# Performance work log

Measured on AMD Instinct MI355X. Metric: run time of the kernel, lower is better.

Reference implementation:

```python
import jax, jax.numpy as jnp
import numpy as np

N_NODES = 100000
N_EDGES = 1600000
IN_SIZE, HID_SIZE, OUT_SIZE = 128, 64, 64


def _glorot(key, shape):
    lim = float(np.sqrt(6.0 / (shape[0] + shape[1])))
    return jax.random.uniform(key, shape, jnp.float32, -lim, lim)


def setup_inputs() -> dict:
    key = jax.random.key(0)
    ks = jax.random.split(key, 6)
    features = jax.random.normal(ks[0], (N_NODES, IN_SIZE), jnp.float32)
    src = jax.random.randint(ks[1], (N_EDGES,), 0, N_NODES)
    dst = jax.random.randint(ks[2], (N_EDGES,), 0, N_NODES)
    return {
        "features": features,
        "W0": _glorot(ks[3], (IN_SIZE, HID_SIZE)),
        "b0": jnp.zeros((HID_SIZE,), jnp.float32),
        "W1": _glorot(ks[4], (HID_SIZE, HID_SIZE)),
        "b1": jnp.zeros((HID_SIZE,), jnp.float32),
        "W2": _glorot(ks[5], (HID_SIZE, OUT_SIZE)),
        "b2": jnp.zeros((OUT_SIZE,), jnp.float32),
        "src": src,
        "dst": dst,
    }


def reference(features, W0, b0, W1, b1, W2, b2, src, dst):
    # DGL GraphConv with norm='both': h' = relu(D_in^{-1/2} A D_out^{-1/2} h W + b)
    # Dropout layers are identity in eval mode (deterministic baseline).
    N = features.shape[0]
    ones = jnp.ones(src.shape, features.dtype)
    deg_out = jax.ops.segment_sum(ones, src, num_segments=N)
    deg_in = jax.ops.segment_sum(ones, dst, num_segments=N)
    norm_src = jnp.where(deg_out > 0, deg_out, 1.0) ** -0.5  # [N]
    norm_dst = jnp.where(deg_in > 0, deg_in, 1.0) ** -0.5    # [N]

    def layer(h, W, b):
        h = h * norm_src[:, None]          # source-side degree norm
        m = (h @ W)[src]                   # project first (in >= out), then gather [E, d_out]
        agg = jax.ops.segment_sum(m, dst, num_segments=N)  # scatter-add to destinations
        return jax.nn.relu(agg * norm_dst[:, None] + b)

    h = layer(features, W0, b0)
    h = layer(h, W1, b1)
    return layer(h, W2, b2)
```

## Files before the change

### kernel.cpp

```cpp
#include <hip/hip_runtime.h>
#include <hip/hip_bf16.h>

typedef __hip_bfloat16 bf16;
typedef __attribute__((ext_vector_type(8))) short bf16x8;
typedef __attribute__((ext_vector_type(8))) unsigned short u16x8;
typedef __attribute__((ext_vector_type(4))) float f32x4;
typedef __attribute__((ext_vector_type(4))) int i32x4;
typedef __attribute__((ext_vector_type(4))) short s16x4;

__device__ __forceinline__ float b2f(unsigned short u) {
  return __uint_as_float(((unsigned)u) << 16);
}
__device__ __forceinline__ unsigned short f2b(float x) {
  bf16 h = __float2bfloat16(x);
  return *reinterpret_cast<unsigned short*>(&h);
}

__global__ void k_passA(const int* __restrict__ src, const int* __restrict__ dst, int E,
                        int nbuck, int M, int* __restrict__ counts,
                        const unsigned short* __restrict__ raw, int* __restrict__ flag) {
  if (blockIdx.x == 256) {
    __shared__ int sbad, snz;
    const int t = threadIdx.x;
    if (t == 0) { sbad = 0; snz = 0; }
    __syncthreads();
    const unsigned short u = raw[t];
    const float a = fabsf(b2f(u));
    if (!(a < 100.f)) atomicAdd(&sbad, 1);
    if (((t & 1) == 0) && u != 0) atomicAdd(&snz, 1);
    __syncthreads();
    if (t == 0) flag[0] = (sbad == 0 && snz > 0) ? 1 : 0;
    return;
  }
  extern __shared__ int lh[];
  int* lh1 = lh;
  int* lh2 = lh + nbuck;
  const int t = threadIdx.x;
  for (int k = t; k < 2 * nbuck; k += 256) lh[k] = 0;
  __syncthreads();
  const int chunk = (E + 255) / 256;
  const int s = blockIdx.x * chunk;
  const int e = min(E, s + chunk);
  for (int i = s + t; i < e; i += 256) {
    atomicAdd(&lh1[dst[i] >> 8], 1);
    atomicAdd(&lh2[src[i] >> 8], 1);
  }
  __syncthreads();
  for (int k = t; k < nbuck; k += 256) {
    counts[k * 256 + blockIdx.x] = lh1[k];
    counts[M + k * 256 + blockIdx.x] = lh2[k];
  }
}

__global__ void k_scan1(const int* __restrict__ a, int M2, int* __restrict__ bsums) {
  __shared__ int sdata[256];
  int i = blockIdx.x * 256 + threadIdx.x;
  int v = (i < M2) ? a[i] : 0;
  sdata[threadIdx.x] = v;
  __syncthreads();
  for (int s = 128; s > 0; s >>= 1) {
    if (threadIdx.x < s) sdata[threadIdx.x] += sdata[threadIdx.x + s];
    __syncthreads();
  }
  if (threadIdx.x == 0) bsums[blockIdx.x] = sdata[0];
}

__global__ void k_scan2(int* __restrict__ bsums, int nb, int* __restrict__ rowStart,
                        int N, int E) {
  __shared__ int s[1024];
  const int t = threadIdx.x;
  const int v = (t < nb) ? bsums[t] : 0;
  s[t] = v;
  __syncthreads();
  for (int off = 1; off < 1024; off <<= 1) {
    int u = (t >= off) ? s[t - off] : 0;
    __syncthreads();
    s[t] += u;
    __syncthreads();
  }
  if (t < nb) bsums[t] = s[t] - v;
  if (t == 0) rowStart[N] = E;
}

__global__ void k_scan3(int* __restrict__ a, int M2, const int* __restrict__ bsums) {
  __shared__ int sdata[256];
  int i = blockIdx.x * 256 + threadIdx.x;
  int v = (i < M2) ? a[i] : 0;
  sdata[threadIdx.x] = v;
  __syncthreads();
  for (int off = 1; off < 256; off <<= 1) {
    int t = (threadIdx.x >= off) ? sdata[threadIdx.x - off] : 0;
    __syncthreads();
    sdata[threadIdx.x] += t;
    __syncthreads();
  }
  if (i < M2) a[i] = bsums[blockIdx.x] + sdata[threadIdx.x] - v;
}

__global__ void k_passC(const int* __restrict__ src, const int* __restrict__ dst, int E,
                        int nbuck, int M, const int* __restrict__ S,
                        int* __restrict__ tmp, unsigned char* __restrict__ tmp2) {
  extern __shared__ int cur[];
  int* cur1 = cur;
  int* cur2 = cur + nbuck;
  const int t = threadIdx.x;
  for (int k = t; k < nbuck; k += 256) {
    cur1[k] = S[k * 256 + blockIdx.x];
    cur2[k] = S[M + k * 256 + blockIdx.x];
  }
  __syncthreads();
  const int chunk = (E + 255) / 256;
  const int s = blockIdx.x * chunk;
  const int e = min(E, s + chunk);
  for (int i = s + t; i < e; i += 256) {
    const int sv = src[i];
    const int d = dst[i];
    const int pos1 = atomicAdd(&cur1[d >> 8], 1);
    tmp[pos1] = sv | ((d & 255) << 20);
    const int pos2 = atomicAdd(&cur2[sv >> 8], 1);
    tmp2[pos2 - E] = (unsigned char)(sv & 255);
  }
}

__global__ void k_passD(const int* __restrict__ tmp, const unsigned char* __restrict__ tmp2,
                        const int* __restrict__ S, int nbuck, int M, int N, int E,
                        int* __restrict__ rowStart, int* __restrict__ edgeSrc,
                        float* __restrict__ ns, float* __restrict__ nd) {
  __shared__ int h[256];
  __shared__ int ex[256];
  __shared__ int c[256];
  const int t = threadIdx.x;
  const int k = blockIdx.x;
  const int node = k * 256 + t;
  const int bs2 = S[M + k * 256] - E;
  const int be2 = (k + 1 < nbuck) ? (S[M + (k + 1) * 256] - E) : E;
  h[t] = 0;
  __syncthreads();
  for (int i = bs2 + t; i < be2; i += 256) atomicAdd(&h[tmp2[i]], 1);
  __syncthreads();
  if (node < N) {
    int dov = h[t];
    if (dov <= 0) dov = 1;
    ns[node] = rsqrtf((float)dov);
  }
  __syncthreads();
  const int bs = S[k * 256];
  const int be = (k + 1 < nbuck) ? S[(k + 1) * 256] : E;
  h[t] = 0;
  __syncthreads();
  for (int i = bs + t; i < be; i += 256) atomicAdd(&h[tmp[i] >> 20], 1);
  __syncthreads();
  const int cnt = h[t];
  ex[t] = cnt;
  __syncthreads();
  for (int off = 1; off < 256; off <<= 1) {
    int u = (t >= off) ? ex[t - off] : 0;
    __syncthreads();
    ex[t] += u;
    __syncthreads();
  }
  const int excl = ex[t] - cnt;
  if (node < N) {
    rowStart[node] = bs + excl;
    nd[node] = rsqrtf((float)(cnt > 0 ? cnt : 1));
  }
  c[t] = bs + excl;
  __syncthreads();
  for (int i = bs + t; i < be; i += 256) {
    const int v = tmp[i];
    const int pos = atomicAdd(&c[v >> 20], 1);
    edgeSrc[pos] = v & 0xFFFFF;
  }
}

__global__ void k_prepW(const void* __restrict__ W0, const void* __restrict__ W1,
                        const void* __restrict__ W2, const int* __restrict__ flag,
                        unsigned short* __restrict__ WT0, unsigned short* __restrict__ WT1,
                        unsigned short* __restrict__ WT2) {
  const bool isb = (*flag != 0);
  const int i = blockIdx.x * 256 + threadIdx.x;
  if (i < 8192) {
    const int n = i >> 7, k = i & 127;
    const float v = isb ? b2f(((const unsigned short*)W0)[k * 64 + n])
                        : ((const float*)W0)[k * 64 + n];
    WT0[i] = f2b(v);
  } else if (i < 12288) {
    const int j = i - 8192;
    const int n = j >> 6, k = j & 63;
    const float v = isb ? b2f(((const unsigned short*)W1)[k * 64 + n])
                        : ((const float*)W1)[k * 64 + n];
    WT1[j] = f2b(v);
  } else if (i < 16384) {
    const int j = i - 12288;
    const int n = j >> 6, k = j & 63;
    const float v = isb ? b2f(((const unsigned short*)W2)[k * 64 + n])
                        : ((const float*)W2)[k * 64 + n];
    WT2[j] = f2b(v);
  }
}

template <int K, bool FIRST, bool SCALE>
__device__ __forceinline__ void gemm_loadA(const void* hin, bool isb, int rowA,
                                           int quad, bf16x8* A) {
  constexpr int KT = K / 32;
  if (FIRST && !isb) {
    const float* hp = (const float*)hin + (size_t)rowA * K;
#pragma unroll
    for (int kt = 0; kt < KT; ++kt) {
      const float4 u0 = *(const float4*)(hp + kt * 32 + quad * 8);
      const float4 u1 = *(const float4*)(hp + kt * 32 + quad * 8 + 4);
      A[kt][0] = (short)f2b(u0.x); A[kt][1] = (short)f2b(u0.y);
      A[kt][2] = (short)f2b(u0.z); A[kt][3] = (short)f2b(u0.w);
      A[kt][4] = (short)f2b(u1.x); A[kt][5] = (short)f2b(u1.y);
      A[kt][6] = (short)f2b(u1.z); A[kt][7] = (short)f2b(u1.w);
    }
  } else {
    const unsigned short* hp = (const unsigned short*)hin + (size_t)rowA * K;
#pragma unroll
    for (int kt = 0; kt < KT; ++kt)
      A[kt] = *(const bf16x8*)(hp + kt * 32 + quad * 8);
  }
}

template <int K, bool FIRST, bool SCALE>
__global__ void __launch_bounds__(256) k_gemm(
    const void* __restrict__ hin, const unsigned short* __restrict__ WT,
    const int* __restrict__ flag, const float* __restrict__ norm_src,
    int N, unsigned short* __restrict__ out) {
  constexpr int KT = K / 32;
  constexpr int CST = 72;
  __shared__ unsigned short Cl[4][16 * CST];
  const bool isb = (*flag != 0);
  const int tid = threadIdx.x;
  const int lane = tid & 63;
  const int quad = lane >> 4;
  const int l16 = lane & 15;
  const int w = tid >> 6;
  unsigned short* myC = &Cl[w][0];

  bf16x8 Bf[KT][4];
#pragma unroll
  for (int kt = 0; kt < KT; ++kt)
#pragma unroll
    for (int nt = 0; nt < 4; ++nt)
      Bf[kt][nt] = *(const bf16x8*)(WT + (size_t)(nt * 16 + l16) * K + kt * 32 + quad * 8);

  const int wid = blockIdx.x * 4 + w;
  const int nw = gridDim.x * 4;
  const int G = (N + 15) >> 4;

  bf16x8 A0[KT], A1[KT];
  if (wid < G) {
    int r0 = (wid << 4) + l16;
    if (r0 >= N) r0 = N - 1;
    gemm_loadA<K, FIRST, SCALE>(hin, isb, r0, quad, A0);
  }
  for (int g = wid; g < G; g += nw) {
    if (g + nw < G) {
      int r1 = ((g + nw) << 4) + l16;
      if (r1 >= N) r1 = N - 1;
      gemm_loadA<K, FIRST, SCALE>(hin, isb, r1, quad, A1);
    }
    f32x4 acc[4] = {{0.f, 0.f, 0.f, 0.f}, {0.f, 0.f, 0.f, 0.f},
                    {0.f, 0.f, 0.f, 0.f}, {0.f, 0.f, 0.f, 0.f}};
#pragma unroll
    for (int kt = 0; kt < KT; ++kt) {
#pragma unroll
      for (int nt = 0; nt < 4; ++nt)
        acc[nt] = __builtin_amdgcn_mfma_f32_16x16x32_bf16(A0[kt], Bf[kt][nt], acc[nt], 0, 0, 0);
    }
    const int rowD = quad * 4;
#pragma unroll
    for (int r = 0; r < 4; ++r) {
      const int nodeW = (g << 4) + rowD + r;
      const float f = (SCALE && nodeW < N) ? norm_src[nodeW] : 1.0f;
#pragma unroll
      for (int nt = 0; nt < 4; ++nt)
        myC[(rowD + r) * CST + nt * 16 + l16] = f2b(SCALE ? acc[nt][r] * f : acc[nt][r]);
    }
    const int row2 = lane >> 2;
    const int c0 = (lane & 3) * 16;
    const int node = (g << 4) + row2;
    if (node < N) {
      const u16x8 v0 = *(const u16x8*)&myC[row2 * CST + c0];
      const u16x8 v1 = *(const u16x8*)&myC[row2 * CST + c0 + 8];
      *(u16x8*)(out + (size_t)node * 64 + c0) = v0;
      *(u16x8*)(out + (size_t)node * 64 + c0 + 8) = v1;
    }
#pragma unroll
    for (int kt = 0; kt < KT; ++kt) A0[kt] = A1[kt];
  }
}

__device__ __forceinline__ void agg_chunk_compute(unsigned trbase, int cb32, int lo,
                                                  unsigned span, int quad, f32x4* acc) {
  const int posbase = cb32 + (quad << 2);
  const unsigned u0 = (unsigned)(posbase - lo);
  bf16x8 Af;
#pragma unroll
  for (int j = 0; j < 8; ++j) {
    const unsigned off = (j < 4) ? (unsigned)j : (unsigned)(12 + j);
    Af[j] = ((u0 + off) < span) ? (short)0x3F80 : (short)0;
  }
  s16x4 t0[4], t1[4];
#pragma unroll
  for (int nt = 0; nt < 4; ++nt) {
    const unsigned a = trbase + (unsigned)(nt * 1024);
    asm volatile("ds_read_b64_tr_b16 %0, %1" : "=v"(t0[nt]) : "v"(a) : "memory");
    asm volatile("ds_read_b64_tr_b16 %0, %1 offset:512" : "=v"(t1[nt]) : "v"(a) : "memory");
  }
  asm volatile("s_waitcnt lgkmcnt(0)" ::: "memory");
  __builtin_amdgcn_sched_barrier(0);
#pragma unroll
  for (int nt = 0; nt < 4; ++nt) {
    bf16x8 Bf;
    Bf[0] = t0[nt][0]; Bf[1] = t0[nt][1]; Bf[2] = t0[nt][2]; Bf[3] = t0[nt][3];
    Bf[4] = t1[nt][0]; Bf[5] = t1[nt][1]; Bf[6] = t1[nt][2]; Bf[7] = t1[nt][3];
    acc[nt] = __builtin_amdgcn_mfma_f32_16x16x32_bf16(Af, Bf, acc[nt], 0, 0, 0);
  }
}

template <bool LAST>
__global__ void __launch_bounds__(256) k_aggregate(
    const unsigned short* __restrict__ proj,
    const int* __restrict__ edgeSrc, const int* __restrict__ rowStart,
    const float* __restrict__ norm_dst, const float* __restrict__ norm_src,
    const void* __restrict__ bias, const int* __restrict__ flag,
    int N, int E, void* __restrict__ outp) {
  __shared__ unsigned short lds[4][2048];
  const bool isb = (*flag != 0);
  const int tid = threadIdx.x;
  const int w = tid >> 6;
  const int lane = tid & 63;
  const int l16 = lane & 15;
  const int quad = lane >> 4;
  const int e32 = lane & 31;
  const int p = lane >> 5;

  const int wid = blockIdx.x * 4 + w;
  const int g0 = wid * 8;

  float bcol[4];
#pragma unroll
  for (int nt = 0; nt < 4; ++nt) {
    const int col = nt * 16 + l16;
    bcol[nt] = isb ? b2f(((const unsigned short*)bias)[col]) : ((const float*)bias)[col];
  }

  const int cb = rowStart[min(g0, N)];
  const int ce = rowStart[min(g0 + 8, N)];
  const int L = ce - cb;
  const int nch = (L + 31) >> 5;

  const int rsi = min(g0 + min(l16, 8), N);
  const int rsj = min(g0 + min(l16 + 1, 8), N);
  const int lo = rowStart[rsi];
  const unsigned span = (unsigned)(rowStart[rsj] - lo);

  int idxc[6];
#pragma unroll
  for (int t = 0; t < 6; ++t) {
    const int pos = min(cb + t * 32 + e32, E - 1);
    idxc[t] = edgeSrc[pos];
  }

  unsigned short* myl = &lds[w][0];
  unsigned wofs[4];
#pragma unroll
  for (int q = 0; q < 4; ++q) {
    const int n0 = p * 32 + q * 8;
    wofs[q] = (unsigned)((n0 >> 4) * 512 + e32 * 16 + (n0 & 15));
  }
  const unsigned trbase = (unsigned)(uintptr_t)myl + (unsigned)lane * 8u;

  f32x4 acc[4] = {{0.f, 0.f, 0.f, 0.f}, {0.f, 0.f, 0.f, 0.f},
                  {0.f, 0.f, 0.f, 0.f}, {0.f, 0.f, 0.f, 0.f}};

  i32x4 gb[4][4];
#define AGG_ISSUE(t, b)                                                         \
  {                                                                             \
    const unsigned short* rp = proj + (size_t)idxc[t] * 64 + p * 32;            \
    gb[b][0] = *(const i32x4*)(rp);                                             \
    gb[b][1] = *(const i32x4*)(rp + 8);                                         \
    gb[b][2] = *(const i32x4*)(rp + 16);                                        \
    gb[b][3] = *(const i32x4*)(rp + 24);                                        \
  }
  if (0 < nch) AGG_ISSUE(0, 0);
  if (1 < nch) AGG_ISSUE(1, 1);
  if (2 < nch) AGG_ISSUE(2, 2);
  if (3 < nch) AGG_ISSUE(3, 3);

#pragma unroll
  for (int tt = 0; tt < 6; ++tt) {
    if (tt < nch) {
#pragma unroll
      for (int q = 0; q < 4; ++q) *(i32x4*)(myl + wofs[q]) = gb[tt & 3][q];
      if (tt + 4 < 6 && tt + 4 < nch) AGG_ISSUE(tt + 4, tt & 3);
      asm volatile("s_waitcnt lgkmcnt(0)" ::: "memory");
      agg_chunk_compute(trbase, cb + tt * 32, lo, span, quad, acc);
    }
  }
  for (int t = 6; t < nch; ++t) {
    const int pos = min(cb + t * 32 + e32, E - 1);
    const int idx = edgeSrc[pos];
    const unsigned short* rp = proj + (size_t)idx * 64 + p * 32;
    i32x4 g4[4];
    g4[0] = *(const i32x4*)(rp);
    g4[1] = *(const i32x4*)(rp + 8);
    g4[2] = *(const i32x4*)(rp + 16);
    g4[3] = *(const i32x4*)(rp + 24);
#pragma unroll
    for (int q = 0; q < 4; ++q) *(i32x4*)(myl + wofs[q]) = g4[q];
    asm volatile("s_waitcnt lgkmcnt(0)" ::: "memory");
    agg_chunk_compute(trbase, cb + t * 32, lo, span, quad, acc);
  }
#undef AGG_ISSUE

  if (LAST && !isb) {
    float* fs = (float*)myl;
#pragma unroll
    for (int reg = 0; reg < 4; ++reg) {
      const int row = quad * 4 + reg;
      if (row < 8) {
        const int node = min(g0 + row, N - 1);
        const float nd = norm_dst[node];
#pragma unroll
        for (int nt = 0; nt < 4; ++nt)
          fs[row * 64 + nt * 16 + l16] = fmaxf(fmaf(acc[nt][reg], nd, bcol[nt]), 0.f);
      }
    }
    asm volatile("s_waitcnt lgkmcnt(0)" ::: "memory");
    __builtin_amdgcn_sched_barrier(0);
    const int r = lane >> 3;
    const int c0 = (lane & 7) * 8;
    const int node = g0 + r;
    if (node < N) {
      const float4 v0 = *(const float4*)&fs[r * 64 + c0];
      const float4 v1 = *(const float4*)&fs[r * 64 + c0 + 4];
      float* of = (float*)outp + (size_t)node * 64 + c0;
      *(float4*)of = v0;
      *(float4*)(of + 4) = v1;
    }
  } else {
#pragma unroll
    for (int reg = 0; reg < 4; ++reg) {
      const int row = quad * 4 + reg;
      if (row < 8) {
        const int node = min(g0 + row, N - 1);
        const float nd = norm_dst[node];
        const float esc = LAST ? 1.f : norm_src[node];
#pragma unroll
        for (int nt = 0; nt < 4; ++nt) {
          float x = fmaxf(fmaf(acc[nt][reg], nd, bcol[nt]), 0.f);
          if (!LAST) x *= esc;
          myl[row * 64 + nt * 16 + l16] = f2b(x);
        }
      }
    }
    asm volatile("s_waitcnt lgkmcnt(0)" ::: "memory");
    __builtin_amdgcn_sched_barrier(0);
    if (lane < 32) {
      const int r = lane >> 2;
      const int c0 = (lane & 3) * 16;
      const int node = g0 + r;
      if (node < N) {
        const u16x8 v0 = *(const u16x8*)&myl[r * 64 + c0];
        const u16x8 v1 = *(const u16x8*)&myl[r * 64 + c0 + 8];
        *(u16x8*)((unsigned short*)outp + (size_t)node * 64 + c0) = v0;
        *(u16x8*)((unsigned short*)outp + (size_t)node * 64 + c0 + 8) = v1;
      }
    }
  }
}

extern "C" void kernel_launch(void* const* d_in, const int* in_sizes, int n_in,
                              void* d_out, int out_size, void* d_ws, size_t ws_size,
                              hipStream_t stream) {
  const void* features = d_in[0];
  const void* W0 = d_in[1];
  const void* b0 = d_in[2];
  const void* W1 = d_in[3];
  const void* b1 = d_in[4];
  const void* W2 = d_in[5];
  const void* b2 = d_in[6];
  const int* src = (const int*)d_in[7];
  const int* dst = (const int*)d_in[8];
  const int N = in_sizes[0] / 128;
  const int E = in_sizes[7];
  const int NBUCK = (N + 255) >> 8;
  const int M = NBUCK * 256;
  const int M2 = 2 * M;

  char* w = (char*)d_ws;
  size_t off = 0;
  auto alloc = [&](size_t bytes) {
    void* p = w + off;
    off = (off + bytes + 255) & ~(size_t)255;
    return p;
  };
  int* flag = (int*)alloc(4);
  int* rowStart = (int*)alloc((size_t)(N + 1) * 4);
  int* counts = (int*)alloc((size_t)M2 * 4);
  int* bsums = (int*)alloc(1024 * 4);
  float* norm_src = (float*)alloc((size_t)N * 4);
  float* norm_dst = (float*)alloc((size_t)N * 4);
  int* tmp = (int*)alloc((size_t)E * 4);
  unsigned char* tmp2 = (unsigned char*)alloc((size_t)E);
  int* edgeSrc = (int*)alloc((size_t)E * 4);
  unsigned short* projA = (unsigned short*)alloc((size_t)N * 64 * 2);
  unsigned short* WT0 = (unsigned short*)alloc(64 * 128 * 2);
  unsigned short* WT1 = (unsigned short*)alloc(64 * 64 * 2);
  unsigned short* WT2 = (unsigned short*)alloc(64 * 64 * 2);
  unsigned short* hB = (unsigned short*)d_out;

  const size_t lds_nb = (size_t)NBUCK * 2 * 4;
  const int G16 = (N + 15) / 16;
  const int GB = (G16 + 7) / 8;

  k_passA<<<257, 256, lds_nb, stream>>>(src, dst, E, NBUCK, M, counts,
                                        (const unsigned short*)features, flag);
  const int NB2 = (M2 + 255) / 256;
  k_scan1<<<NB2, 256, 0, stream>>>(counts, M2, bsums);
  k_scan2<<<1, 1024, 0, stream>>>(bsums, NB2, rowStart, N, E);
  k_scan3<<<NB2, 256, 0, stream>>>(counts, M2, bsums);
  k_passC<<<256, 256, lds_nb, stream>>>(src, dst, E, NBUCK, M, counts, tmp, tmp2);
  k_passD<<<NBUCK, 256, 0, stream>>>(tmp, tmp2, counts, NBUCK, M, N, E,
                                     rowStart, edgeSrc, norm_src, norm_dst);
  k_prepW<<<64, 256, 0, stream>>>(W0, W1, W2, flag, WT0, WT1, WT2);

  const int AB = (((N + 7) / 8) + 3) / 4;
  k_gemm<128, true, true><<<GB, 256, 0, stream>>>(features, WT0, flag, norm_src, N, projA);
  k_aggregate<false><<<AB, 256, 0, stream>>>(projA, edgeSrc, rowStart, norm_dst, norm_src, b0, flag, N, E, hB);
  k_gemm<64, false, false><<<GB, 256, 0, stream>>>(hB, WT1, flag, nullptr, N, projA);
  k_aggregate<false><<<AB, 256, 0, stream>>>(projA, edgeSrc, rowStart, norm_dst, norm_src, b1, flag, N, E, hB);
  k_gemm<64, false, false><<<GB, 256, 0, stream>>>(hB, WT2, flag, nullptr, N, projA);
  k_aggregate<true><<<AB, 256, 0, stream>>>(projA, edgeSrc, rowStart, norm_dst, norm_src, b2, flag, N, E, d_out);
}
```

Measured before the change: 335.3 us.

## Fuse weight transpose into GEMM via LDS and shrink aggregate gather prefetch depth

Drops the separate weight-prep kernel. Each GEMM block now loads and converts its weight matrix into a padded, transposed LDS tile and reads B fragments from LDS per MFMA instead of holding them in registers. This saves a kernel launch and workspace buffers, and frees registers, but every block repeats the weight load and each MFMA step adds LDS reads. Separately, the aggregate kernel's gather prefetch ring goes from 4 to 2 buffers to lower register pressure, at the cost of less memory latency hiding.

Measured after the change: 315.4 us. 1.06x faster.

```diff
diff --git a/kernel.cpp b/kernel.cpp
--- a/kernel.cpp
+++ b/kernel.cpp
@@ -173,32 +173,6 @@
   }
 }
 
-__global__ void k_prepW(const void* __restrict__ W0, const void* __restrict__ W1,
-                        const void* __restrict__ W2, const int* __restrict__ flag,
-                        unsigned short* __restrict__ WT0, unsigned short* __restrict__ WT1,
-                        unsigned short* __restrict__ WT2) {
-  const bool isb = (*flag != 0);
-  const int i = blockIdx.x * 256 + threadIdx.x;
-  if (i < 8192) {
-    const int n = i >> 7, k = i & 127;
-    const float v = isb ? b2f(((const unsigned short*)W0)[k * 64 + n])
-                        : ((const float*)W0)[k * 64 + n];
-    WT0[i] = f2b(v);
-  } else if (i < 12288) {
-    const int j = i - 8192;
-    const int n = j >> 6, k = j & 63;
-    const float v = isb ? b2f(((const unsigned short*)W1)[k * 64 + n])
-                        : ((const float*)W1)[k * 64 + n];
-    WT1[j] = f2b(v);
-  } else if (i < 16384) {
-    const int j = i - 12288;
-    const int n = j >> 6, k = j & 63;
-    const float v = isb ? b2f(((const unsigned short*)W2)[k * 64 + n])
-                        : ((const float*)W2)[k * 64 + n];
-    WT2[j] = f2b(v);
-  }
-}
-
 template <int K, bool FIRST, bool SCALE>
 __device__ __forceinline__ void gemm_loadA(const void* hin, bool isb, int rowA,
                                            int quad, bf16x8* A) {
@@ -224,27 +198,46 @@
 
 template <int K, bool FIRST, bool SCALE>
 __global__ void __launch_bounds__(256) k_gemm(
-    const void* __restrict__ hin, const unsigned short* __restrict__ WT,
+    const void* __restrict__ hin, const void* __restrict__ Wv,
     const int* __restrict__ flag, const float* __restrict__ norm_src,
     int N, unsigned short* __restrict__ out) {
   constexpr int KT = K / 32;
+  constexpr int ST = K + 8;
   constexpr int CST = 72;
+  __shared__ unsigned short Wl[64 * ST];
   __shared__ unsigned short Cl[4][16 * CST];
   const bool isb = (*flag != 0);
   const int tid = threadIdx.x;
+
+  {
+    const unsigned short* Wus = (const unsigned short*)Wv;
+    const float* Wf = (const float*)Wv;
+    for (int i0 = tid * 8; i0 < K * 64; i0 += 2048) {
+      const int k = i0 >> 6;
+      const int n0 = i0 & 63;
+      unsigned short v[8];
+      if (isb) {
+        const u16x8 u = *(const u16x8*)(Wus + i0);
+#pragma unroll
+        for (int j = 0; j < 8; ++j) v[j] = u[j];
+      } else {
+        const float4 f0 = *(const float4*)(Wf + i0);
+        const float4 f1 = *(const float4*)(Wf + i0 + 4);
+        v[0] = f2b(f0.x); v[1] = f2b(f0.y); v[2] = f2b(f0.z); v[3] = f2b(f0.w);
+        v[4] = f2b(f1.x); v[5] = f2b(f1.y); v[6] = f2b(f1.z); v[7] = f2b(f1.w);
+      }
+#pragma unroll
+      for (int j = 0; j < 8; ++j) Wl[(n0 + j) * ST + k] = v[j];
+    }
+  }
+  __syncthreads();
+
   const int lane = tid & 63;
   const int quad = lane >> 4;
   const int l16 = lane & 15;
   const int w = tid >> 6;
   unsigned short* myC = &Cl[w][0];
 
-  bf16x8 Bf[KT][4];
-#pragma unroll
-  for (int kt = 0; kt < KT; ++kt)
-#pragma unroll
-    for (int nt = 0; nt < 4; ++nt)
-      Bf[kt][nt] = *(const bf16x8*)(WT + (size_t)(nt * 16 + l16) * K + kt * 32 + quad * 8);
-
   const int wid = blockIdx.x * 4 + w;
   const int nw = gridDim.x * 4;
   const int G = (N + 15) >> 4;
@@ -265,9 +258,12 @@
                     {0.f, 0.f, 0.f, 0.f}, {0.f, 0.f, 0.f, 0.f}};
 #pragma unroll
     for (int kt = 0; kt < KT; ++kt) {
-#pragma unroll
-      for (int nt = 0; nt < 4; ++nt)
-        acc[nt] = __builtin_amdgcn_mfma_f32_16x16x32_bf16(A0[kt], Bf[kt][nt], acc[nt], 0, 0, 0);
+      const int koff = kt * 32 + quad * 8;
+#pragma unroll
+      for (int nt = 0; nt < 4; ++nt) {
+        const bf16x8 Bf = *(const bf16x8*)&Wl[(nt * 16 + l16) * ST + koff];
+        acc[nt] = __builtin_amdgcn_mfma_f32_16x16x32_bf16(A0[kt], Bf, acc[nt], 0, 0, 0);
+      }
     }
     const int rowD = quad * 4;
 #pragma unroll
@@ -376,7 +372,7 @@
   f32x4 acc[4] = {{0.f, 0.f, 0.f, 0.f}, {0.f, 0.f, 0.f, 0.f},
                   {0.f, 0.f, 0.f, 0.f}, {0.f, 0.f, 0.f, 0.f}};
 
-  i32x4 gb[4][4];
+  i32x4 gb[2][4];
 #define AGG_ISSUE(t, b)                                                         \
   {                                                                             \
     const unsigned short* rp = proj + (size_t)idxc[t] * 64 + p * 32;            \
@@ -387,15 +383,13 @@
   }
   if (0 < nch) AGG_ISSUE(0, 0);
   if (1 < nch) AGG_ISSUE(1, 1);
-  if (2 < nch) AGG_ISSUE(2, 2);
-  if (3 < nch) AGG_ISSUE(3, 3);
 
 #pragma unroll
   for (int tt = 0; tt < 6; ++tt) {
     if (tt < nch) {
 #pragma unroll
-      for (int q = 0; q < 4; ++q) *(i32x4*)(myl + wofs[q]) = gb[tt & 3][q];
-      if (tt + 4 < 6 && tt + 4 < nch) AGG_ISSUE(tt + 4, tt & 3);
+      for (int q = 0; q < 4; ++q) *(i32x4*)(myl + wofs[q]) = gb[tt & 1][q];
+      if (tt + 2 < 6 && tt + 2 < nch) AGG_ISSUE(tt + 2, tt & 1);
       asm volatile("s_waitcnt lgkmcnt(0)" ::: "memory");
       agg_chunk_compute(trbase, cb + tt * 32, lo, span, quad, acc);
     }
@@ -508,9 +502,6 @@
   unsigned char* tmp2 = (unsigned char*)alloc((size_t)E);
   int* edgeSrc = (int*)alloc((size_t)E * 4);
   unsigned short* projA = (unsigned short*)alloc((size_t)N * 64 * 2);
-  unsigned short* WT0 = (unsigned short*)alloc(64 * 128 * 2);
-  unsigned short* WT1 = (unsigned short*)alloc(64 * 64 * 2);
-  unsigned short* WT2 = (unsigned short*)alloc(64 * 64 * 2);
   unsigned short* hB = (unsigned short*)d_out;
 
   const size_t lds_nb = (size_t)NBUCK * 2 * 4;
@@ -526,13 +517,12 @@
   k_passC<<<256, 256, lds_nb, stream>>>(src, dst, E, NBUCK, M, counts, tmp, tmp2);
   k_passD<<<NBUCK, 256, 0, stream>>>(tmp, tmp2, counts, NBUCK, M, N, E,
                                      rowStart, edgeSrc, norm_src, norm_dst);
-  k_prepW<<<64, 256, 0, stream>>>(W0, W1, W2, flag, WT0, WT1, WT2);
 
   const int AB = (((N + 7) / 8) + 3) / 4;
-  k_gemm<128, true, true><<<GB, 256, 0, stream>>>(features, WT0, flag, norm_src, N, projA);
+  k_gemm<128, true, true><<<GB, 256, 0, stream>>>(features, W0, flag, norm_src, N, projA);
   k_aggregate<false><<<AB, 256, 0, stream>>>(projA, edgeSrc, rowStart, norm_dst, norm_src, b0, flag, N, E, hB);
-  k_gemm<64, false, false><<<GB, 256, 0, stream>>>(hB, WT1, flag, nullptr, N, projA);
+  k_gemm<64, false, false><<<GB, 256, 0, stream>>>(hB, W1, flag, nullptr, N, projA);
   k_aggregate<false><<<AB, 256, 0, stream>>>(projA, edgeSrc, rowStart, norm_dst, norm_src, b1, flag, N, E, hB);
-  k_gemm<64, false, false><<<GB, 256, 0, stream>>>(hB, WT2, flag, nullptr, N, projA);
+  k_gemm<64, false, false><<<GB, 256, 0, stream>>>(hB, W2, flag, nullptr, N, projA);
   k_aggregate<true><<<AB, 256, 0, stream>>>(projA, edgeSrc, rowStart, norm_dst, norm_src, b2, flag, N, E, d_out);
 }
```
